# Kernel optimization log

Measured on AMD Instinct MI355X. Metric: run time of the kernel, lower is better.

Reference implementation:

```python
import jax, jax.numpy as jnp
import numpy as np

N = 100000
E = 1600000
D_IN = 128
D_HID = 128
D_OUT = 128


def _glorot(key, shape):
    fan_in, fan_out = shape[1], shape[0]
    lim = np.sqrt(6.0 / (fan_in + fan_out)).astype(np.float32)
    return jax.random.uniform(key, shape, jnp.float32, -lim, lim)


def setup_inputs() -> dict:
    key = jax.random.key(0)
    ks = jax.random.split(key, 8)
    x = jax.random.normal(ks[0], (N, D_IN), jnp.float32)
    edge_index = jax.random.randint(ks[1], (2, E), 0, N, jnp.int64)
    # SAGEConv params: lin_l acts on aggregated neighbors (has bias), lin_r on root.
    W1l = _glorot(ks[2], (D_HID, D_IN))
    W1r = _glorot(ks[3], (D_HID, D_IN))
    b1 = jnp.zeros((D_HID,), jnp.float32)
    W2l = _glorot(ks[4], (D_OUT, D_HID))
    W2r = _glorot(ks[5], (D_OUT, D_HID))
    b2 = jnp.zeros((D_OUT,), jnp.float32)
    return {"x": x, "edge_index": edge_index,
            "W1l": W1l, "W1r": W1r, "b1": b1,
            "W2l": W2l, "W2r": W2r, "b2": b2}


def _sage_conv(x, src, dst, Wl, Wr, b):
    # mean-aggregate neighbor features j->i, then lin_l(mean) + lin_r(x) + b
    msgs = x[src]                                             # [E, d]
    summed = jax.ops.segment_sum(msgs, dst, num_segments=N)   # [N, d]
    deg = jax.ops.segment_sum(jnp.ones((src.shape[0],), x.dtype), dst,
                              num_segments=N)                 # [N]
    mean = summed / jnp.maximum(deg, 1.0)[:, None]
    return mean @ Wl.T + x @ Wr.T + b


def reference(x, edge_index, W1l, W1r, b1, W2l, W2r, b2):
    src, dst = edge_index[0], edge_index[1]
    h = jax.nn.relu(_sage_conv(x, src, dst, W1l, W1r, b1))
    # dropout p=0.2 is identity in eval mode
    out = _sage_conv(h, src, dst, W2l, W2r, b2)
    return out
```

## Files before the change

### kernel.cpp

```cpp
#include <hip/hip_runtime.h>
#include <hip/hip_bf16.h>

#define N_NODES 100000
#define N_EDGES 1600000
#define D 128
#define NBUCK 782
#define BSTRIDE 2560
#define EPB 4096

typedef __attribute__((ext_vector_type(8))) short short8v;
typedef __attribute__((ext_vector_type(4))) float f32x4;

__device__ __forceinline__ unsigned short f2bf(float f) {
    unsigned int u = __float_as_uint(f);
    unsigned int r = (u + 0x7fffu + ((u >> 16) & 1u)) >> 16;
    return (unsigned short)r;
}
__device__ __forceinline__ float bf2f(unsigned int lo16) {
    return __uint_as_float(lo16 << 16);
}
__device__ __forceinline__ short8v zero8() {
    short8v z = {0, 0, 0, 0, 0, 0, 0, 0};
    return z;
}
__device__ __forceinline__ short8v cvt8(const float4 p0, const float4 p1) {
    union { __hip_bfloat162 h[4]; short8v s; } u;
    u.h[0] = __float22bfloat162_rn(make_float2(p0.x, p0.y));
    u.h[1] = __float22bfloat162_rn(make_float2(p0.z, p0.w));
    u.h[2] = __float22bfloat162_rn(make_float2(p1.x, p1.y));
    u.h[3] = __float22bfloat162_rn(make_float2(p1.z, p1.w));
    return u.s;
}

__global__ void k_prep(const float* __restrict__ W1l, const float* __restrict__ W1r,
                       const float* __restrict__ W2l, const float* __restrict__ W2r,
                       unsigned short* __restrict__ wc1, unsigned short* __restrict__ wc2,
                       int* __restrict__ gcnt) {
    int idx = blockIdx.x * 256 + threadIdx.x;
    if (idx < 16384)       wc1[idx] = f2bf(W1l[idx]);
    else if (idx < 32768)  wc1[idx] = f2bf(W1r[idx - 16384]);
    else if (idx < 65536) {
        int j = idx - 32768;
        int o = j >> 8, k2 = j & 255;
        float v = (k2 < 128) ? W2l[o * 128 + k2] : W2r[o * 128 + (k2 - 128)];
        wc2[j] = f2bf(v);
    }
    else if (idx - 65536 < NBUCK) gcnt[idx - 65536] = 0;
}

__global__ __launch_bounds__(256) void k_bscatter(const int* __restrict__ src,
                                                  const int* __restrict__ dst,
                                                  int* __restrict__ gcnt,
                                                  unsigned int* __restrict__ ebuf) {
    __shared__ int cnt[NBUCK];
    __shared__ int base[NBUCK];
    const int t = threadIdx.x;
    const int e0 = blockIdx.x * EPB;
    for (int i = t; i < NBUCK; i += 256) cnt[i] = 0;
    __syncthreads();
    unsigned int pay[16];
    int meta[16];
#pragma unroll
    for (int u = 0; u < 16; ++u) {
        int e = e0 + u * 256 + t;
        if (e < N_EDGES) {
            int d = dst[e];
            int b = d >> 7;
            int r = atomicAdd(&cnt[b], 1);
            meta[u] = (b << 16) | r;
            pay[u] = ((unsigned int)(d & 127) << 17) | (unsigned int)src[e];
        } else meta[u] = -1;
    }
    __syncthreads();
    for (int i = t; i < NBUCK; i += 256) {
        int c = cnt[i];
        base[i] = c ? atomicAdd(&gcnt[i], c) : 0;
    }
    __syncthreads();
#pragma unroll
    for (int u = 0; u < 16; ++u) {
        if (meta[u] >= 0) {
            int b = meta[u] >> 16;
            int r = meta[u] & 0xffff;
            ebuf[b * BSTRIDE + base[b] + r] = pay[u];
        }
    }
}

__global__ __launch_bounds__(256) void k_bsort(const unsigned int* __restrict__ ebuf,
                                               const int* __restrict__ gcnt,
                                               int* __restrict__ row_start,
                                               int* __restrict__ ssrc) {
    __shared__ int h[128];
    __shared__ int sc[128];
    const int b = blockIdx.x;
    const int t = threadIdx.x;
    const int eb = b * BSTRIDE;
    const int n = gcnt[b];
    if (t < 128) h[t] = 0;
    __syncthreads();
    unsigned int pay[BSTRIDE / 256];
    int meta[BSTRIDE / 256];
#pragma unroll
    for (int u = 0; u < BSTRIDE / 256; ++u) {
        int e = t + u * 256;
        if (e < n) {
            unsigned int pk = ebuf[eb + e];
            int dl = pk >> 17;
            int r = atomicAdd(&h[dl], 1);
            meta[u] = (dl << 16) | r;
            pay[u] = pk;
        } else meta[u] = -1;
    }
    __syncthreads();
    if (t < 128) sc[t] = h[t];
    __syncthreads();
    for (int o = 1; o < 128; o <<= 1) {
        int add = 0;
        if (t < 128 && t >= o) add = sc[t - o];
        __syncthreads();
        if (t < 128) sc[t] += add;
        __syncthreads();
    }
    if (t < 128) {
        int excl = sc[t] - h[t];
        row_start[b * 129 + t] = eb + excl;
        sc[t] = excl;
    }
    if (t == 0) row_start[b * 129 + 128] = eb + n;
    __syncthreads();
#pragma unroll
    for (int u = 0; u < BSTRIDE / 256; ++u) {
        if (meta[u] >= 0) {
            int dl = meta[u] >> 16;
            int r = meta[u] & 0xffff;
            ssrc[eb + sc[dl] + r] = (int)(pay[u] & 0x1ffffu);
        }
    }
}

__global__ __launch_bounds__(256) void k_gemm1(
    const float* __restrict__ Af,
    const unsigned short* __restrict__ Bt,
    const float* __restrict__ bias,
    unsigned short* __restrict__ Tout,
    unsigned short* __restrict__ Hout)
{
    const int wid = threadIdx.x >> 6;
    const int lane = threadIdx.x & 63;
    const int l15 = lane & 15, lg = lane >> 4;
    const int col_base = wid * 64;

    short8v bfrag[4][4];
#pragma unroll
    for (int cg = 0; cg < 4; ++cg)
#pragma unroll
        for (int ks = 0; ks < 4; ++ks)
            bfrag[cg][ks] = *(const short8v*)&Bt[(size_t)(col_base + cg * 16 + l15) * 128
                                                 + ks * 32 + lg * 8];
    float bv[4];
#pragma unroll
    for (int cg = 0; cg < 4; ++cg)
        bv[cg] = (wid >= 2) ? bias[(wid - 2) * 64 + cg * 16 + l15] : 0.0f;

    const int ntiles = (N_NODES + 63) / 64;
    for (int tile = blockIdx.x; tile < ntiles; tile += gridDim.x) {
        const int row0 = tile * 64;
        f32x4 acc[4][4];
#pragma unroll
        for (int rg = 0; rg < 4; ++rg)
#pragma unroll
            for (int cg = 0; cg < 4; ++cg)
                acc[rg][cg] = (f32x4){0.f, 0.f, 0.f, 0.f};

#pragma unroll
        for (int rg = 0; rg < 4; ++rg) {
            const int arow = row0 + rg * 16 + l15;
            short8v afrag[4];
            if (arow < N_NODES) {
#pragma unroll
                for (int ks = 0; ks < 4; ++ks)
                    afrag[ks] = cvt8(*(const float4*)&Af[(size_t)arow * 128 + ks * 32 + lg * 8],
                                     *(const float4*)&Af[(size_t)arow * 128 + ks * 32 + lg * 8 + 4]);
            } else {
#pragma unroll
                for (int ks = 0; ks < 4; ++ks) afrag[ks] = zero8();
            }
#pragma unroll
            for (int cg = 0; cg < 4; ++cg)
#pragma unroll
                for (int ks = 0; ks < 4; ++ks)
                    acc[rg][cg] = __builtin_amdgcn_mfma_f32_16x16x32_bf16(
                        afrag[ks], bfrag[cg][ks], acc[rg][cg], 0, 0, 0);
        }

        unsigned short* outp = (wid < 2) ? Tout : Hout;
        const int cb = (wid < 2) ? col_base : col_base - 128;
        const bool addb = (wid >= 2);
#pragma unroll
        for (int rg = 0; rg < 4; ++rg) {
            const int rbase = row0 + rg * 16 + lg * 4;
#pragma unroll
            for (int cg = 0; cg < 4; ++cg) {
                const int col = cb + cg * 16 + l15;
#pragma unroll
                for (int i = 0; i < 4; ++i) {
                    int row = rbase + i;
                    if (row < N_NODES) {
                        float v = acc[rg][cg][i] + (addb ? bv[cg] : 0.0f);
                        outp[(size_t)row * 128 + col] = f2bf(v);
                    }
                }
            }
        }
    }
}

__global__ __launch_bounds__(256) void k_gemm2(
    const unsigned short* __restrict__ M,
    const unsigned short* __restrict__ H,
    const unsigned short* __restrict__ Bt,
    const float* __restrict__ bias,
    float* __restrict__ out)
{
    const int wid = threadIdx.x >> 6;
    const int lane = threadIdx.x & 63;
    const int l15 = lane & 15, lg = lane >> 4;
    const int col_base = wid * 32;

    short8v bfrag[2][8];
#pragma unroll
    for (int cg = 0; cg < 2; ++cg)
#pragma unroll
        for (int ks = 0; ks < 8; ++ks)
            bfrag[cg][ks] = *(const short8v*)&Bt[(size_t)(col_base + cg * 16 + l15) * 256
                                                 + ks * 32 + lg * 8];
    float bv[2];
#pragma unroll
    for (int cg = 0; cg < 2; ++cg)
        bv[cg] = bias[col_base + cg * 16 + l15];

    const int ntiles = (N_NODES + 63) / 64;
    for (int tile = blockIdx.x; tile < ntiles; tile += gridDim.x) {
        const int row0 = tile * 64;
        f32x4 acc[4][2];
#pragma unroll
        for (int rg = 0; rg < 4; ++rg)
#pragma unroll
            for (int cg = 0; cg < 2; ++cg)
                acc[rg][cg] = (f32x4){0.f, 0.f, 0.f, 0.f};

#pragma unroll
        for (int rg = 0; rg < 4; ++rg) {
            const int arow = row0 + rg * 16 + l15;
            short8v afrag[8];
            if (arow < N_NODES) {
#pragma unroll
                for (int ks = 0; ks < 4; ++ks) {
                    afrag[ks]     = *(const short8v*)&M[(size_t)arow * 128 + ks * 32 + lg * 8];
                    afrag[ks + 4] = *(const short8v*)&H[(size_t)arow * 128 + ks * 32 + lg * 8];
                }
            } else {
#pragma unroll
                for (int ks = 0; ks < 8; ++ks) afrag[ks] = zero8();
            }
#pragma unroll
            for (int cg = 0; cg < 2; ++cg)
#pragma unroll
                for (int ks = 0; ks < 8; ++ks)
                    acc[rg][cg] = __builtin_amdgcn_mfma_f32_16x16x32_bf16(
                        afrag[ks], bfrag[cg][ks], acc[rg][cg], 0, 0, 0);
        }

#pragma unroll
        for (int rg = 0; rg < 4; ++rg) {
            const int rbase = row0 + rg * 16 + lg * 4;
#pragma unroll
            for (int cg = 0; cg < 2; ++cg) {
                const int col = col_base + cg * 16 + l15;
#pragma unroll
                for (int i = 0; i < 4; ++i) {
                    int row = rbase + i;
                    if (row < N_NODES)
                        out[(size_t)row * 128 + col] = acc[rg][cg][i] + bv[cg];
                }
            }
        }
    }
}

template <bool RMW>
__global__ __launch_bounds__(256) void k_agg(
    const unsigned short* __restrict__ t_mat,
    const int* __restrict__ ssrc,
    const int* __restrict__ row_start,
    unsigned short* __restrict__ io)
{
    int w = (blockIdx.x * blockDim.x + threadIdx.x) >> 6;
    int lane = threadIdx.x & 63;
    if (w >= N_NODES) return;
    const int b = w >> 7, dl = w & 127;
    const int rs = row_start[b * 129 + dl];
    const int re = row_start[b * 129 + dl + 1];
    const int d = re - rs;
    const int half = lane >> 5;
    const int l31 = lane & 31;

    uint2 cur;
    cur.x = 0u; cur.y = 0u;
    if (RMW && lane < 32)
        cur = *((const uint2*)io + (size_t)w * 32 + l31);

    const uint2* tlane = (const uint2*)t_mat + l31;
    float a0 = 0.f, a1 = 0.f, a2 = 0.f, a3 = 0.f;

    for (int q0 = rs; q0 < re; q0 += 64) {
        int nb = 0;
        if (q0 + lane < re) nb = ssrc[q0 + lane];
        const int m = min(64, re - q0);
        int q = 0;
        for (; q + 16 <= m; q += 16) {
            uint2 v[8];
#pragma unroll
            for (int u = 0; u < 8; ++u) {
                int j = __shfl(nb, q + u * 2 + half);
                v[u] = tlane[(size_t)j * 32];
            }
#pragma unroll
            for (int u = 0; u < 8; ++u) {
                a0 += bf2f(v[u].x & 0xffffu);
                a1 += __uint_as_float(v[u].x & 0xffff0000u);
                a2 += bf2f(v[u].y & 0xffffu);
                a3 += __uint_as_float(v[u].y & 0xffff0000u);
            }
        }
        for (; q + 2 <= m; q += 2) {
            int j = __shfl(nb, q + half);
            uint2 vv = tlane[(size_t)j * 32];
            a0 += bf2f(vv.x & 0xffffu);
            a1 += __uint_as_float(vv.x & 0xffff0000u);
            a2 += bf2f(vv.y & 0xffffu);
            a3 += __uint_as_float(vv.y & 0xffff0000u);
        }
        if (q < m) {
            int j = __shfl(nb, q);
            if (half == 0) {
                uint2 vv = tlane[(size_t)j * 32];
                a0 += bf2f(vv.x & 0xffffu);
                a1 += __uint_as_float(vv.x & 0xffff0000u);
                a2 += bf2f(vv.y & 0xffffu);
                a3 += __uint_as_float(vv.y & 0xffff0000u);
            }
        }
    }

    a0 += __shfl_xor(a0, 32);
    a1 += __shfl_xor(a1, 32);
    a2 += __shfl_xor(a2, 32);
    a3 += __shfl_xor(a3, 32);

    if (lane < 32) {
        const float inv = 1.0f / (float)max(d, 1);
        float r0, r1, r2, r3;
        if (RMW) {
            r0 = fmaxf(bf2f(cur.x & 0xffffu) + inv * a0, 0.f);
            r1 = fmaxf(__uint_as_float(cur.x & 0xffff0000u) + inv * a1, 0.f);
            r2 = fmaxf(bf2f(cur.y & 0xffffu) + inv * a2, 0.f);
            r3 = fmaxf(__uint_as_float(cur.y & 0xffff0000u) + inv * a3, 0.f);
        } else {
            r0 = inv * a0; r1 = inv * a1; r2 = inv * a2; r3 = inv * a3;
        }
        uint2 o;
        o.x = (unsigned int)f2bf(r0) | ((unsigned int)f2bf(r1) << 16);
        o.y = (unsigned int)f2bf(r2) | ((unsigned int)f2bf(r3) << 16);
        *((uint2*)io + (size_t)w * 32 + l31) = o;
    }
}


extern "C" void kernel_launch(void* const* d_in, const int* in_sizes, int n_in,
                              void* d_out, int out_size, void* d_ws, size_t ws_size,
                              hipStream_t stream) {
    const float* x   = (const float*)d_in[0];
    const int*   ei  = (const int*)d_in[1];
    const float* W1l = (const float*)d_in[2];
    const float* W1r = (const float*)d_in[3];
    const float* b1  = (const float*)d_in[4];
    const float* W2l = (const float*)d_in[5];
    const float* W2r = (const float*)d_in[6];
    const float* b2  = (const float*)d_in[7];
    float* out = (float*)d_out;

    const int* src = ei;
    const int* dst = ei + N_EDGES;

    char* p = (char*)d_ws;
    auto alloc = [&](size_t bytes) {
        char* r = p;
        p += (bytes + 255) & ~(size_t)255;
        return r;
    };
    unsigned short* tb = (unsigned short*)alloc((size_t)N_NODES * D * 2);
    unsigned short* hx = (unsigned short*)alloc((size_t)N_NODES * D * 2);
    unsigned int*   ebuf = (unsigned int*)alloc((size_t)NBUCK * BSTRIDE * 4);
    int*   ssrc      = (int*)alloc((size_t)NBUCK * BSTRIDE * 4);
    int*   gcnt      = (int*)alloc(NBUCK * sizeof(int));
    int*   row_start = (int*)alloc((size_t)NBUCK * 129 * sizeof(int));
    unsigned short* wc1 = (unsigned short*)alloc(256 * 128 * 2);
    unsigned short* wc2 = (unsigned short*)alloc(128 * 256 * 2);

    const int agg_grid = (N_NODES + 3) / 4;

    k_prep<<<(65536 + NBUCK + 255) / 256, 256, 0, stream>>>(W1l, W1r, W2l, W2r, wc1, wc2, gcnt);
    k_bscatter<<<(N_EDGES + EPB - 1) / EPB, 256, 0, stream>>>(src, dst, gcnt, ebuf);
    k_bsort<<<NBUCK, 256, 0, stream>>>(ebuf, gcnt, row_start, ssrc);

    k_gemm1<<<640, 256, 0, stream>>>(x, wc1, b1, tb, hx);
    k_agg<true><<<agg_grid, 256, 0, stream>>>(tb, ssrc, row_start, hx);

    k_agg<false><<<agg_grid, 256, 0, stream>>>(hx, ssrc, row_start, tb);
    k_gemm2<<<640, 256, 0, stream>>>(tb, hx, wc2, b2, out);
}
```

Before: 247.6 us.

## Fuse second-layer mean aggregation into the second GEMM via LDS staging

Replaces the separate second aggregation kernel and the second GEMM with one kernel. Each block aggregates 64 nodes' neighbor means into shared memory, then runs the MFMA GEMM directly from LDS plus the root features. This removes a global write and re-read of the N×128 bf16 intermediate and one kernel launch. In exchange each wave now walks 16 nodes serially, which may hide gather latency less well, and weight fragments are reloaded for every tile instead of once per persistent block.

```diff
diff --git a/kernel.cpp b/kernel.cpp
--- a/kernel.cpp
+++ b/kernel.cpp
@@ -7,6 +7,7 @@
 #define NBUCK 782
 #define BSTRIDE 2560
 #define EPB 4096
+#define M2S 136
 
 typedef __attribute__((ext_vector_type(8))) short short8v;
 typedef __attribute__((ext_vector_type(4))) float f32x4;
@@ -216,81 +217,7 @@
     }
 }
 
-__global__ __launch_bounds__(256) void k_gemm2(
-    const unsigned short* __restrict__ M,
-    const unsigned short* __restrict__ H,
-    const unsigned short* __restrict__ Bt,
-    const float* __restrict__ bias,
-    float* __restrict__ out)
-{
-    const int wid = threadIdx.x >> 6;
-    const int lane = threadIdx.x & 63;
-    const int l15 = lane & 15, lg = lane >> 4;
-    const int col_base = wid * 32;
-
-    short8v bfrag[2][8];
-#pragma unroll
-    for (int cg = 0; cg < 2; ++cg)
-#pragma unroll
-        for (int ks = 0; ks < 8; ++ks)
-            bfrag[cg][ks] = *(const short8v*)&Bt[(size_t)(col_base + cg * 16 + l15) * 256
-                                                 + ks * 32 + lg * 8];
-    float bv[2];
-#pragma unroll
-    for (int cg = 0; cg < 2; ++cg)
-        bv[cg] = bias[col_base + cg * 16 + l15];
-
-    const int ntiles = (N_NODES + 63) / 64;
-    for (int tile = blockIdx.x; tile < ntiles; tile += gridDim.x) {
-        const int row0 = tile * 64;
-        f32x4 acc[4][2];
-#pragma unroll
-        for (int rg = 0; rg < 4; ++rg)
-#pragma unroll
-            for (int cg = 0; cg < 2; ++cg)
-                acc[rg][cg] = (f32x4){0.f, 0.f, 0.f, 0.f};
-
-#pragma unroll
-        for (int rg = 0; rg < 4; ++rg) {
-            const int arow = row0 + rg * 16 + l15;
-            short8v afrag[8];
-            if (arow < N_NODES) {
-#pragma unroll
-                for (int ks = 0; ks < 4; ++ks) {
-                    afrag[ks]     = *(const short8v*)&M[(size_t)arow * 128 + ks * 32 + lg * 8];
-                    afrag[ks + 4] = *(const short8v*)&H[(size_t)arow * 128 + ks * 32 + lg * 8];
-                }
-            } else {
-#pragma unroll
-                for (int ks = 0; ks < 8; ++ks) afrag[ks] = zero8();
-            }
-#pragma unroll
-            for (int cg = 0; cg < 2; ++cg)
-#pragma unroll
-                for (int ks = 0; ks < 8; ++ks)
-                    acc[rg][cg] = __builtin_amdgcn_mfma_f32_16x16x32_bf16(
-                        afrag[ks], bfrag[cg][ks], acc[rg][cg], 0, 0, 0);
-        }
-
-#pragma unroll
-        for (int rg = 0; rg < 4; ++rg) {
-            const int rbase = row0 + rg * 16 + lg * 4;
-#pragma unroll
-            for (int cg = 0; cg < 2; ++cg) {
-                const int col = col_base + cg * 16 + l15;
-#pragma unroll
-                for (int i = 0; i < 4; ++i) {
-                    int row = rbase + i;
-                    if (row < N_NODES)
-                        out[(size_t)row * 128 + col] = acc[rg][cg][i] + bv[cg];
-                }
-            }
-        }
-    }
-}
-
-template <bool RMW>
-__global__ __launch_bounds__(256) void k_agg(
+__global__ __launch_bounds__(256) void k_agg1(
     const unsigned short* __restrict__ t_mat,
     const int* __restrict__ ssrc,
     const int* __restrict__ row_start,
@@ -308,7 +235,7 @@
 
     uint2 cur;
     cur.x = 0u; cur.y = 0u;
-    if (RMW && lane < 32)
+    if (lane < 32)
         cur = *((const uint2*)io + (size_t)w * 32 + l31);
 
     const uint2* tlane = (const uint2*)t_mat + l31;
@@ -361,19 +288,148 @@
 
     if (lane < 32) {
         const float inv = 1.0f / (float)max(d, 1);
-        float r0, r1, r2, r3;
-        if (RMW) {
-            r0 = fmaxf(bf2f(cur.x & 0xffffu) + inv * a0, 0.f);
-            r1 = fmaxf(__uint_as_float(cur.x & 0xffff0000u) + inv * a1, 0.f);
-            r2 = fmaxf(bf2f(cur.y & 0xffffu) + inv * a2, 0.f);
-            r3 = fmaxf(__uint_as_float(cur.y & 0xffff0000u) + inv * a3, 0.f);
-        } else {
-            r0 = inv * a0; r1 = inv * a1; r2 = inv * a2; r3 = inv * a3;
-        }
+        float r0 = fmaxf(bf2f(cur.x & 0xffffu) + inv * a0, 0.f);
+        float r1 = fmaxf(__uint_as_float(cur.x & 0xffff0000u) + inv * a1, 0.f);
+        float r2 = fmaxf(bf2f(cur.y & 0xffffu) + inv * a2, 0.f);
+        float r3 = fmaxf(__uint_as_float(cur.y & 0xffff0000u) + inv * a3, 0.f);
         uint2 o;
         o.x = (unsigned int)f2bf(r0) | ((unsigned int)f2bf(r1) << 16);
         o.y = (unsigned int)f2bf(r2) | ((unsigned int)f2bf(r3) << 16);
         *((uint2*)io + (size_t)w * 32 + l31) = o;
+    }
+}
+
+__global__ __launch_bounds__(256) void k_agg_gemm2(
+    const unsigned short* __restrict__ H,
+    const int* __restrict__ ssrc,
+    const int* __restrict__ row_start,
+    const unsigned short* __restrict__ Bt,
+    const float* __restrict__ bias,
+    float* __restrict__ out)
+{
+    __shared__ unsigned short m2s[64 * M2S];
+    const int wid = threadIdx.x >> 6;
+    const int lane = threadIdx.x & 63;
+    const int l15 = lane & 15, lg = lane >> 4;
+    const int half = lane >> 5, l31 = lane & 31;
+    const int row0 = blockIdx.x * 64;
+
+    const int col_base = wid * 32;
+    short8v bfrag[2][8];
+#pragma unroll
+    for (int cg = 0; cg < 2; ++cg)
+#pragma unroll
+        for (int ks = 0; ks < 8; ++ks)
+            bfrag[cg][ks] = *(const short8v*)&Bt[(size_t)(col_base + cg * 16 + l15) * 256
+                                                 + ks * 32 + lg * 8];
+    float bv[2];
+#pragma unroll
+    for (int cg = 0; cg < 2; ++cg)
+        bv[cg] = bias[col_base + cg * 16 + l15];
+
+    const uint2* tlane = (const uint2*)H + l31;
+    for (int tt = 0; tt < 16; ++tt) {
+        const int n = row0 + wid * 16 + tt;
+        const int bb = n >> 7, dl = n & 127;
+        const int rs = row_start[bb * 129 + dl];
+        const int re = row_start[bb * 129 + dl + 1];
+        float a0 = 0.f, a1 = 0.f, a2 = 0.f, a3 = 0.f;
+        for (int q0 = rs; q0 < re; q0 += 64) {
+            int nb = 0;
+            if (q0 + lane < re) nb = ssrc[q0 + lane];
+            const int m = min(64, re - q0);
+            int q = 0;
+            for (; q + 16 <= m; q += 16) {
+                uint2 v[8];
+#pragma unroll
+                for (int u = 0; u < 8; ++u) {
+                    int j = __shfl(nb, q + u * 2 + half);
+                    v[u] = tlane[(size_t)j * 32];
+                }
+#pragma unroll
+                for (int u = 0; u < 8; ++u) {
+                    a0 += bf2f(v[u].x & 0xffffu);
+                    a1 += __uint_as_float(v[u].x & 0xffff0000u);
+                    a2 += bf2f(v[u].y & 0xffffu);
+                    a3 += __uint_as_float(v[u].y & 0xffff0000u);
+                }
+            }
+            for (; q + 2 <= m; q += 2) {
+                int j = __shfl(nb, q + half);
+                uint2 vv = tlane[(size_t)j * 32];
+                a0 += bf2f(vv.x & 0xffffu);
+                a1 += __uint_as_float(vv.x & 0xffff0000u);
+                a2 += bf2f(vv.y & 0xffffu);
+                a3 += __uint_as_float(vv.y & 0xffff0000u);
+            }
+            if (q < m) {
+                int j = __shfl(nb, q);
+                if (half == 0) {
+                    uint2 vv = tlane[(size_t)j * 32];
+                    a0 += bf2f(vv.x & 0xffffu);
+                    a1 += __uint_as_float(vv.x & 0xffff0000u);
+                    a2 += bf2f(vv.y & 0xffffu);
+                    a3 += __uint_as_float(vv.y & 0xffff0000u);
+                }
+            }
+        }
+        a0 += __shfl_xor(a0, 32);
+        a1 += __shfl_xor(a1, 32);
+        a2 += __shfl_xor(a2, 32);
+        a3 += __shfl_xor(a3, 32);
+        if (lane < 32) {
+            const float inv = 1.0f / (float)max(re - rs, 1);
+            uint2 o;
+            o.x = (unsigned int)f2bf(inv * a0) | ((unsigned int)f2bf(inv * a1) << 16);
+            o.y = (unsigned int)f2bf(inv * a2) | ((unsigned int)f2bf(inv * a3) << 16);
+            *(uint2*)&m2s[(wid * 16 + tt) * M2S + l31 * 4] = o;
+        }
+    }
+    __syncthreads();
+
+    f32x4 acc[4][2];
+#pragma unroll
+    for (int rg = 0; rg < 4; ++rg)
+#pragma unroll
+        for (int cg = 0; cg < 2; ++cg)
+            acc[rg][cg] = (f32x4){0.f, 0.f, 0.f, 0.f};
+
+#pragma unroll
+    for (int rg = 0; rg < 4; ++rg) {
+        const int arow = row0 + rg * 16 + l15;
+        short8v afrag[8];
+#pragma unroll
+        for (int ks = 0; ks < 4; ++ks)
+            afrag[ks] = *(const short8v*)&m2s[(rg * 16 + l15) * M2S + ks * 32 + lg * 8];
+        if (arow < N_NODES) {
+#pragma unroll
+            for (int ks = 0; ks < 4; ++ks)
+                afrag[ks + 4] = *(const short8v*)&H[(size_t)arow * 128 + ks * 32 + lg * 8];
+        } else {
+#pragma unroll
+            for (int ks = 0; ks < 4; ++ks) afrag[ks + 4] = zero8();
+        }
+#pragma unroll
+        for (int cg = 0; cg < 2; ++cg)
+#pragma unroll
+            for (int ks = 0; ks < 8; ++ks)
+                acc[rg][cg] = __builtin_amdgcn_mfma_f32_16x16x32_bf16(
+                    afrag[ks], bfrag[cg][ks], acc[rg][cg], 0, 0, 0);
+    }
+
+#pragma unroll
+    for (int rg = 0; rg < 4; ++rg) {
+        const int rbase = row0 + rg * 16 + lg * 4;
+#pragma unroll
+        for (int cg = 0; cg < 2; ++cg) {
+            const int col = col_base + cg * 16 + l15;
+#pragma unroll
+            for (int i = 0; i < 4; ++i) {
+                int row = rbase + i;
+                if (row < N_NODES)
+                    out[(size_t)row * 128 + col] = acc[rg][cg][i] + bv[cg];
+            }
+        }
     }
 }
 
@@ -410,14 +466,14 @@
     unsigned short* wc2 = (unsigned short*)alloc(128 * 256 * 2);
 
     const int agg_grid = (N_NODES + 3) / 4;
+    const int tiles = (N_NODES + 63) / 64;
 
     k_prep<<<(65536 + NBUCK + 255) / 256, 256, 0, stream>>>(W1l, W1r, W2l, W2r, wc1, wc2, gcnt);
     k_bscatter<<<(N_EDGES + EPB - 1) / EPB, 256, 0, stream>>>(src, dst, gcnt, ebuf);
     k_bsort<<<NBUCK, 256, 0, stream>>>(ebuf, gcnt, row_start, ssrc);
 
     k_gemm1<<<640, 256, 0, stream>>>(x, wc1, b1, tb, hx);
-    k_agg<true><<<agg_grid, 256, 0, stream>>>(tb, ssrc, row_start, hx);
-
-    k_agg<false><<<agg_grid, 256, 0, stream>>>(hx, ssrc, row_start, tb);
-    k_gemm2<<<640, 256, 0, stream>>>(tb, hx, wc2, b2, out);
-}
+    k_agg1<<<agg_grid, 256, 0, stream>>>(tb, ssrc, row_start, hx);
+
+    k_agg_gemm2<<<tiles, 256, 0, stream>>>(hx, ssrc, row_start, wc2, b2, out);
+}
```

Measured after the change: 301.9 us. +21.9%, slower.
